# Kernel optimization log

Hardware: AMD Instinct MI355X
Metric: run time of the kernel (lower is better)

The kernel has to match this reference:

```python
import jax, jax.numpy as jnp
import numpy as np

B, T, H = 32, 2048, 1024


def setup_inputs() -> dict:
    key = jax.random.key(0)
    k1, k2, k3, k4, k5 = jax.random.split(key, 5)
    hidden = jax.random.normal(k1, (1, B, H), dtype=jnp.float32)
    encoder_outputs = jax.random.normal(k2, (B, T, H), dtype=jnp.float32)
    # nn.Linear(2H, H): weight [H, 2H], bias [H]
    lim = 1.0 / np.sqrt(2 * H)
    W = jax.random.uniform(k3, (H, 2 * H), minval=-lim, maxval=lim, dtype=jnp.float32)
    b = jax.random.uniform(k4, (H,), minval=-lim, maxval=lim, dtype=jnp.float32)
    stdv = 1.0 / np.sqrt(H)
    v = jax.random.uniform(k5, (H,), minval=-stdv, maxval=stdv, dtype=jnp.float32)
    return {"hidden": hidden, "encoder_outputs": encoder_outputs, "W": W, "b": b, "v": v}


def reference(hidden, encoder_outputs, W, b, v):
    # hidden: [1, B, H] -> broadcast to [B, T, H]
    h = jnp.broadcast_to(jnp.transpose(hidden, (1, 0, 2)), encoder_outputs.shape)
    x = jnp.concatenate([h, encoder_outputs], axis=2)          # [B, T, 2H]
    energy = jnp.tanh(jnp.einsum('btd,hd->bth', x, W) + b)      # [B, T, H]
    scores = jnp.einsum('h,bth->bt', v, energy)[:, None, :]     # [B, 1, T]
    return jax.nn.softmax(scores, axis=2)
```

## Files before the change

kernel.cpp:

```cpp
#include <hip/hip_runtime.h>
#include <hip/hip_bf16.h>

#define H 1024
#define T 2048
#define B 32
#define BK 128
#define NCHUNK 8

typedef __attribute__((ext_vector_type(8))) __bf16 bf16x8;
typedef __attribute__((ext_vector_type(16))) float f32x16;
typedef __attribute__((ext_vector_type(8))) unsigned short u16x8;

__device__ __forceinline__ unsigned short f2bf(float f) {
    unsigned int x = __float_as_uint(f);
    x += 0x7fffu + ((x >> 16) & 1u);
    return (unsigned short)(x >> 16);
}

__device__ __forceinline__ float fast_tanh(float x) {
    float t = __expf(2.0f * x);
    return 1.0f - 2.0f * __builtin_amdgcn_rcpf(t + 1.0f);
}

__global__ __launch_bounds__(256) void prep_w_kernel(const float* __restrict__ W,
                                                     unsigned short* __restrict__ Wp) {
    int gid = blockIdx.x * 256 + threadIdx.x;
    int n = gid & (H - 1);
    int kg = gid >> 10;
    const float* srcp = W + (size_t)n * (2 * H) + H + kg * 8;
    float4 f0 = *(const float4*)(srcp);
    float4 f1 = *(const float4*)(srcp + 4);
    u16x8 o;
    o[0] = f2bf(f0.x); o[1] = f2bf(f0.y); o[2] = f2bf(f0.z); o[3] = f2bf(f0.w);
    o[4] = f2bf(f1.x); o[5] = f2bf(f1.y); o[6] = f2bf(f1.z); o[7] = f2bf(f1.w);
    *(u16x8*)(Wp + (size_t)gid * 8) = o;
}

__global__ __launch_bounds__(128) void prep_hp_kernel(const float* __restrict__ hidden,
                                                      const float* __restrict__ W,
                                                      const float* __restrict__ bias,
                                                      float* __restrict__ hp) {
    int b = blockIdx.y;
    int h = blockIdx.x * 128 + threadIdx.x;
    const float* hid = hidden + (size_t)b * H;
    const float* wr = W + (size_t)h * (2 * H);
    float acc = 0.f;
    for (int d = 0; d < H; d += 4) {
        float4 wv = *(const float4*)(wr + d);
        float4 hv = *(const float4*)(hid + d);
        acc += wv.x * hv.x + wv.y * hv.y + wv.z * hv.z + wv.w * hv.w;
    }
    hp[(size_t)b * H + h] = acc + bias[h];
}

__global__ __launch_bounds__(1024, 4) void energy_kernel(const float* __restrict__ enc,
                                                         const float* __restrict__ hp,
                                                         const float* __restrict__ vvec,
                                                         const unsigned short* __restrict__ Wp,
                                                         float* __restrict__ scores) {
    __shared__ __align__(16) unsigned short Abuf[2][NCHUNK * 1024];
    __shared__ float scpart[16][64];

    const int tid = threadIdx.x;
    const int b = blockIdx.y;
    const int t0 = blockIdx.x * 64;
    const int wave = tid >> 6;
    const int lane = tid & 63;
    const int l31 = lane & 31;
    const int hi = lane >> 5;

    const int st_row = tid >> 4;
    const int st_ks = tid & 15;
    const float* st_src = enc + ((size_t)b * T + t0 + st_row) * H + st_ks * 8;
    char* st_dst = (char*)&Abuf[0][0] + st_ks * 1024 + ((st_row ^ (st_ks & 7)) * 16);

    const char* Abase = (const char*)&Abuf[0][0];
    const int l31x = l31;

    const unsigned short* wp_col = Wp + (size_t)(wave * 64 + l31) * 8 + (size_t)hi * (H * 8);

    f32x16 acc[2][2];
#pragma unroll
    for (int rg = 0; rg < 2; ++rg)
#pragma unroll
        for (int cg = 0; cg < 2; ++cg)
#pragma unroll
            for (int i = 0; i < 16; ++i) acc[rg][cg][i] = 0.f;

    {
        float4 f0 = *(const float4*)(st_src + 0);
        float4 f1 = *(const float4*)(st_src + 4);
        u16x8 o;
        o[0] = f2bf(f0.x); o[1] = f2bf(f0.y); o[2] = f2bf(f0.z); o[3] = f2bf(f0.w);
        o[4] = f2bf(f1.x); o[5] = f2bf(f1.y); o[6] = f2bf(f1.z); o[7] = f2bf(f1.w);
        *(u16x8*)(st_dst) = o;
    }
    __syncthreads();

    for (int j = 0; j < NCHUNK; ++j) {
        float4 f0, f1;
        const bool pf = (j < NCHUNK - 1);
        if (pf) {
            const float* p = st_src + (j + 1) * BK;
            f0 = *(const float4*)(p + 0);
            f1 = *(const float4*)(p + 4);
        }
        const char* Ab = Abase + (j & 1) * 16384;
        const unsigned short* wpj = wp_col + (size_t)(j * 16) * (H * 8);
#pragma unroll
        for (int ki = 0; ki < 8; ++ki) {
            const int kslot = ki * 2 + hi;
            const char* ap = Ab + kslot * 1024 + ((l31x ^ (kslot & 7)) * 16);
            bf16x8 a0 = *(const bf16x8*)(ap);
            bf16x8 a1 = *(const bf16x8*)(ap + 512);
            const unsigned short* wpk = wpj + (size_t)(ki * 2) * (H * 8);
            bf16x8 b0 = *(const bf16x8*)(wpk + 0 * 256);
            bf16x8 b1 = *(const bf16x8*)(wpk + 1 * 256);
            acc[0][0] = __builtin_amdgcn_mfma_f32_32x32x16_bf16(a0, b0, acc[0][0], 0, 0, 0);
            acc[0][1] = __builtin_amdgcn_mfma_f32_32x32x16_bf16(a0, b1, acc[0][1], 0, 0, 0);
            acc[1][0] = __builtin_amdgcn_mfma_f32_32x32x16_bf16(a1, b0, acc[1][0], 0, 0, 0);
            acc[1][1] = __builtin_amdgcn_mfma_f32_32x32x16_bf16(a1, b1, acc[1][1], 0, 0, 0);
        }
        if (pf) {
            u16x8 o;
            o[0] = f2bf(f0.x); o[1] = f2bf(f0.y); o[2] = f2bf(f0.z); o[3] = f2bf(f0.w);
            o[4] = f2bf(f1.x); o[5] = f2bf(f1.y); o[6] = f2bf(f1.z); o[7] = f2bf(f1.w);
            *(u16x8*)(st_dst + ((j + 1) & 1) * 16384) = o;
        }
        __syncthreads();
    }

    float pscore[2][16];
#pragma unroll
    for (int rg = 0; rg < 2; ++rg)
#pragma unroll
        for (int r = 0; r < 16; ++r) pscore[rg][r] = 0.f;

    const size_t bH = (size_t)b * H;
#pragma unroll
    for (int cg = 0; cg < 2; ++cg) {
        const int col = wave * 64 + cg * 32 + l31;
        const float hpv = hp[bH + col];
        const float vv = vvec[col];
#pragma unroll
        for (int rg = 0; rg < 2; ++rg)
#pragma unroll
            for (int r = 0; r < 16; ++r)
                pscore[rg][r] += vv * fast_tanh(acc[rg][cg][r] + hpv);
    }

#pragma unroll
    for (int rg = 0; rg < 2; ++rg)
#pragma unroll
        for (int r = 0; r < 16; ++r) {
            float s = pscore[rg][r];
            s += __shfl_xor(s, 1);
            s += __shfl_xor(s, 2);
            s += __shfl_xor(s, 4);
            s += __shfl_xor(s, 8);
            s += __shfl_xor(s, 16);
            pscore[rg][r] = s;
        }
    if (l31 == 0) {
#pragma unroll
        for (int rg = 0; rg < 2; ++rg)
#pragma unroll
            for (int r = 0; r < 16; ++r) {
                int m = (r & 3) + 8 * (r >> 2) + 4 * hi + rg * 32;
                scpart[wave][m] = pscore[rg][r];
            }
    }
    __syncthreads();
    if (tid < 64) {
        float s = 0.f;
#pragma unroll
        for (int w = 0; w < 16; ++w) s += scpart[w][tid];
        scores[(size_t)b * T + t0 + tid] = s;
    }
}

__global__ __launch_bounds__(256) void softmax_kernel(const float* __restrict__ sc,
                                                      float* __restrict__ out) {
    int b = blockIdx.x;
    int tid = threadIdx.x;
    int wave = tid >> 6, lane = tid & 63;
    const float* row = sc + (size_t)b * T;
    float vals[8];
    float m = -1e30f;
#pragma unroll
    for (int i = 0; i < 8; ++i) { vals[i] = row[tid + 256 * i]; m = fmaxf(m, vals[i]); }
#pragma unroll
    for (int s = 1; s < 64; s <<= 1) m = fmaxf(m, __shfl_xor(m, s));
    __shared__ float red[4];
    __shared__ float red2[4];
    if (lane == 0) red[wave] = m;
    __syncthreads();
    m = fmaxf(fmaxf(red[0], red[1]), fmaxf(red[2], red[3]));
    float sum = 0.f;
#pragma unroll
    for (int i = 0; i < 8; ++i) { vals[i] = expf(vals[i] - m); sum += vals[i]; }
#pragma unroll
    for (int s = 1; s < 64; s <<= 1) sum += __shfl_xor(sum, s);
    if (lane == 0) red2[wave] = sum;
    __syncthreads();
    sum = red2[0] + red2[1] + red2[2] + red2[3];
    float inv = 1.0f / sum;
#pragma unroll
    for (int i = 0; i < 8; ++i) out[(size_t)b * T + tid + 256 * i] = vals[i] * inv;
}

extern "C" void kernel_launch(void* const* d_in, const int* in_sizes, int n_in,
                              void* d_out, int out_size, void* d_ws, size_t ws_size,
                              hipStream_t stream) {
    (void)in_sizes; (void)n_in; (void)out_size; (void)ws_size;
    const float* hidden = (const float*)d_in[0];
    const float* enc    = (const float*)d_in[1];
    const float* W      = (const float*)d_in[2];
    const float* bias   = (const float*)d_in[3];
    const float* v      = (const float*)d_in[4];
    float* out = (float*)d_out;

    unsigned short* Wp = (unsigned short*)d_ws;
    float* hp = (float*)((char*)d_ws + 2 * 1024 * 1024);
    float* sc = (float*)((char*)d_ws + 2 * 1024 * 1024 + 128 * 1024);

    prep_w_kernel<<<dim3(512), dim3(256), 0, stream>>>(W, Wp);
    prep_hp_kernel<<<dim3(8, B), dim3(128), 0, stream>>>(hidden, W, bias, hp);
    energy_kernel<<<dim3(T / 64, B), dim3(1024), 0, stream>>>(enc, hp, v, Wp, sc);
    softmax_kernel<<<dim3(B), dim3(256), 0, stream>>>(sc, out);
}
```

Measured before the change: 244.2 us.

## Retile energy GEMM to 128-row blocks split across two column halves

The energy kernel now processes 128 time rows per block and only half the hidden columns (512), with a third grid dimension for the column split. Each wave owns one 32-column slice and four row groups, so each B fragment loaded from global memory is reused across four MFMAs and is software-prefetched two steps ahead. The K chunk shrinks to 64 with 16 iterations. Partial scores from the two column halves are written separately and summed in the softmax kernel. The trade-off is that each encoder tile is converted and staged twice (once per column half) in exchange for larger M reuse and register-pipelined weight loads.

```diff
diff --git a/kernel.cpp b/kernel.cpp
--- a/kernel.cpp
+++ b/kernel.cpp
@@ -4,8 +4,11 @@
 #define H 1024
 #define T 2048
 #define B 32
-#define BK 128
-#define NCHUNK 8
+#define BM 128
+#define BKC 64
+#define NCHUNK 16
+#define NCOLT 2
+#define BCOLS 512
 
 typedef __attribute__((ext_vector_type(8))) __bf16 bf16x8;
 typedef __attribute__((ext_vector_type(16))) float f32x16;
@@ -53,75 +56,86 @@
     hp[(size_t)b * H + h] = acc + bias[h];
 }
 
+#define MFMA32(A, Bv, C) __builtin_amdgcn_mfma_f32_32x32x16_bf16(A, Bv, C, 0, 0, 0)
+
 __global__ __launch_bounds__(1024, 4) void energy_kernel(const float* __restrict__ enc,
                                                          const float* __restrict__ hp,
                                                          const float* __restrict__ vvec,
                                                          const unsigned short* __restrict__ Wp,
-                                                         float* __restrict__ scores) {
-    __shared__ __align__(16) unsigned short Abuf[2][NCHUNK * 1024];
-    __shared__ float scpart[16][64];
+                                                         float* __restrict__ sc_part) {
+    __shared__ __align__(16) unsigned short Abuf[2][BM * BKC];
+    __shared__ float scpart[16][BM];
 
     const int tid = threadIdx.x;
-    const int b = blockIdx.y;
-    const int t0 = blockIdx.x * 64;
+    const int b = blockIdx.z;
+    const int t0 = blockIdx.x * BM;
+    const int c0 = blockIdx.y * BCOLS;
     const int wave = tid >> 6;
     const int lane = tid & 63;
     const int l31 = lane & 31;
     const int hi = lane >> 5;
 
-    const int st_row = tid >> 4;
-    const int st_ks = tid & 15;
+    const int st_ks = tid & 7;
+    const int st_row = tid >> 3;
     const float* st_src = enc + ((size_t)b * T + t0 + st_row) * H + st_ks * 8;
-    char* st_dst = (char*)&Abuf[0][0] + st_ks * 1024 + ((st_row ^ (st_ks & 7)) * 16);
-
-    const char* Abase = (const char*)&Abuf[0][0];
-    const int l31x = l31;
-
-    const unsigned short* wp_col = Wp + (size_t)(wave * 64 + l31) * 8 + (size_t)hi * (H * 8);
-
-    f32x16 acc[2][2];
-#pragma unroll
-    for (int rg = 0; rg < 2; ++rg)
-#pragma unroll
-        for (int cg = 0; cg < 2; ++cg)
-#pragma unroll
-            for (int i = 0; i < 16; ++i) acc[rg][cg][i] = 0.f;
+    char* Ab0 = (char*)&Abuf[0][0];
+    char* st_dst = Ab0 + st_ks * 2048 + (((st_row ^ st_ks)) << 4);
+
+    const unsigned short* wp_base = Wp + (size_t)(c0 + wave * 32 + l31) * 8 + (size_t)hi * (H * 8);
+
+    f32x16 acc[4];
+#pragma unroll
+    for (int rg = 0; rg < 4; ++rg)
+#pragma unroll
+        for (int i = 0; i < 16; ++i) acc[rg][i] = 0.f;
+
+    const int rv0 = 0 * 32 + l31;
+    const int rv1 = 1 * 32 + l31;
+    const int rv2 = 2 * 32 + l31;
+    const int rv3 = 3 * 32 + l31;
 
     {
-        float4 f0 = *(const float4*)(st_src + 0);
+        float4 f0 = *(const float4*)(st_src);
         float4 f1 = *(const float4*)(st_src + 4);
         u16x8 o;
         o[0] = f2bf(f0.x); o[1] = f2bf(f0.y); o[2] = f2bf(f0.z); o[3] = f2bf(f0.w);
         o[4] = f2bf(f1.x); o[5] = f2bf(f1.y); o[6] = f2bf(f1.z); o[7] = f2bf(f1.w);
-        *(u16x8*)(st_dst) = o;
-    }
-    __syncthreads();
+        *(u16x8*)st_dst = o;
+    }
+    bf16x8 bfA = *(const bf16x8*)(wp_base);
+    bf16x8 bfB = *(const bf16x8*)(wp_base + (size_t)1 * (H * 16));
+    __syncthreads();
+
+#define STEP(KI, BF)                                                          \
+    {                                                                          \
+        const int kslot = (KI) * 2 + hi;                                       \
+        const char* ap = Ab + kslot * 2048;                                    \
+        bf16x8 a0 = *(const bf16x8*)(ap + ((rv0 ^ kslot) << 4));               \
+        bf16x8 a1 = *(const bf16x8*)(ap + ((rv1 ^ kslot) << 4));               \
+        bf16x8 a2 = *(const bf16x8*)(ap + ((rv2 ^ kslot) << 4));               \
+        bf16x8 a3 = *(const bf16x8*)(ap + ((rv3 ^ kslot) << 4));               \
+        acc[0] = MFMA32(a0, BF, acc[0]);                                       \
+        acc[1] = MFMA32(a1, BF, acc[1]);                                       \
+        acc[2] = MFMA32(a2, BF, acc[2]);                                       \
+        acc[3] = MFMA32(a3, BF, acc[3]);                                       \
+        const int nit = j * 4 + (KI) + 2;                                      \
+        if (nit < 64) BF = *(const bf16x8*)(wp_base + (size_t)nit * (H * 16)); \
+    }
 
     for (int j = 0; j < NCHUNK; ++j) {
         float4 f0, f1;
-        const bool pf = (j < NCHUNK - 1);
-        if (pf) {
-            const float* p = st_src + (j + 1) * BK;
-            f0 = *(const float4*)(p + 0);
+        const bool pfA = (j < NCHUNK - 1);
+        if (pfA) {
+            const float* p = st_src + (j + 1) * BKC;
+            f0 = *(const float4*)(p);
             f1 = *(const float4*)(p + 4);
         }
-        const char* Ab = Abase + (j & 1) * 16384;
-        const unsigned short* wpj = wp_col + (size_t)(j * 16) * (H * 8);
-#pragma unroll
-        for (int ki = 0; ki < 8; ++ki) {
-            const int kslot = ki * 2 + hi;
-            const char* ap = Ab + kslot * 1024 + ((l31x ^ (kslot & 7)) * 16);
-            bf16x8 a0 = *(const bf16x8*)(ap);
-            bf16x8 a1 = *(const bf16x8*)(ap + 512);
-            const unsigned short* wpk = wpj + (size_t)(ki * 2) * (H * 8);
-            bf16x8 b0 = *(const bf16x8*)(wpk + 0 * 256);
-            bf16x8 b1 = *(const bf16x8*)(wpk + 1 * 256);
-            acc[0][0] = __builtin_amdgcn_mfma_f32_32x32x16_bf16(a0, b0, acc[0][0], 0, 0, 0);
-            acc[0][1] = __builtin_amdgcn_mfma_f32_32x32x16_bf16(a0, b1, acc[0][1], 0, 0, 0);
-            acc[1][0] = __builtin_amdgcn_mfma_f32_32x32x16_bf16(a1, b0, acc[1][0], 0, 0, 0);
-            acc[1][1] = __builtin_amdgcn_mfma_f32_32x32x16_bf16(a1, b1, acc[1][1], 0, 0, 0);
-        }
-        if (pf) {
+        const char* Ab = Ab0 + (j & 1) * 16384;
+        STEP(0, bfA)
+        STEP(1, bfB)
+        STEP(2, bfA)
+        STEP(3, bfB)
+        if (pfA) {
             u16x8 o;
             o[0] = f2bf(f0.x); o[1] = f2bf(f0.y); o[2] = f2bf(f0.z); o[3] = f2bf(f0.w);
             o[4] = f2bf(f1.x); o[5] = f2bf(f1.y); o[6] = f2bf(f1.z); o[7] = f2bf(f1.w);
@@ -129,53 +143,46 @@
         }
         __syncthreads();
     }
-
-    float pscore[2][16];
-#pragma unroll
-    for (int rg = 0; rg < 2; ++rg)
-#pragma unroll
-        for (int r = 0; r < 16; ++r) pscore[rg][r] = 0.f;
+#undef STEP
 
     const size_t bH = (size_t)b * H;
-#pragma unroll
-    for (int cg = 0; cg < 2; ++cg) {
-        const int col = wave * 64 + cg * 32 + l31;
-        const float hpv = hp[bH + col];
-        const float vv = vvec[col];
-#pragma unroll
-        for (int rg = 0; rg < 2; ++rg)
-#pragma unroll
-            for (int r = 0; r < 16; ++r)
-                pscore[rg][r] += vv * fast_tanh(acc[rg][cg][r] + hpv);
-    }
-
-#pragma unroll
-    for (int rg = 0; rg < 2; ++rg)
+    const int col = c0 + wave * 32 + l31;
+    const float hpv = hp[bH + col];
+    const float vv = vvec[col];
+    float psc[4][16];
+#pragma unroll
+    for (int rg = 0; rg < 4; ++rg)
+#pragma unroll
+        for (int r = 0; r < 16; ++r)
+            psc[rg][r] = vv * fast_tanh(acc[rg][r] + hpv);
+
+#pragma unroll
+    for (int rg = 0; rg < 4; ++rg)
 #pragma unroll
         for (int r = 0; r < 16; ++r) {
-            float s = pscore[rg][r];
+            float s = psc[rg][r];
             s += __shfl_xor(s, 1);
             s += __shfl_xor(s, 2);
             s += __shfl_xor(s, 4);
             s += __shfl_xor(s, 8);
             s += __shfl_xor(s, 16);
-            pscore[rg][r] = s;
+            psc[rg][r] = s;
         }
     if (l31 == 0) {
 #pragma unroll
-        for (int rg = 0; rg < 2; ++rg)
+        for (int rg = 0; rg < 4; ++rg)
 #pragma unroll
             for (int r = 0; r < 16; ++r) {
-                int m = (r & 3) + 8 * (r >> 2) + 4 * hi + rg * 32;
-                scpart[wave][m] = pscore[rg][r];
+                int m = rg * 32 + (r & 3) + 8 * (r >> 2) + 4 * hi;
+                scpart[wave][m] = psc[rg][r];
             }
     }
     __syncthreads();
-    if (tid < 64) {
+    if (tid < BM) {
         float s = 0.f;
 #pragma unroll
         for (int w = 0; w < 16; ++w) s += scpart[w][tid];
-        scores[(size_t)b * T + t0 + tid] = s;
+        sc_part[((size_t)blockIdx.y * B + b) * T + t0 + tid] = s;
     }
 }
 
@@ -184,11 +191,16 @@
     int b = blockIdx.x;
     int tid = threadIdx.x;
     int wave = tid >> 6, lane = tid & 63;
-    const float* row = sc + (size_t)b * T;
+    const float* row0 = sc + (size_t)b * T;
+    const float* row1 = sc + ((size_t)B + b) * T;
     float vals[8];
     float m = -1e30f;
 #pragma unroll
-    for (int i = 0; i < 8; ++i) { vals[i] = row[tid + 256 * i]; m = fmaxf(m, vals[i]); }
+    for (int i = 0; i < 8; ++i) {
+        int idx = tid + 256 * i;
+        vals[i] = row0[idx] + row1[idx];
+        m = fmaxf(m, vals[i]);
+    }
 #pragma unroll
     for (int s = 1; s < 64; s <<= 1) m = fmaxf(m, __shfl_xor(m, s));
     __shared__ float red[4];
@@ -226,6 +238,6 @@
 
     prep_w_kernel<<<dim3(512), dim3(256), 0, stream>>>(W, Wp);
     prep_hp_kernel<<<dim3(8, B), dim3(128), 0, stream>>>(hidden, W, bias, hp);
-    energy_kernel<<<dim3(T / 64, B), dim3(1024), 0, stream>>>(enc, hp, v, Wp, sc);
+    energy_kernel<<<dim3(T / BM, NCOLT, B), dim3(1024), 0, stream>>>(enc, hp, v, Wp, sc);
     softmax_kernel<<<dim3(B), dim3(256), 0, stream>>>(sc, out);
 }
```

New measurement: 275.0 us. 12.6% more time.
